# Optimization experiments

Measured on AMD Instinct MI355X. Metric: run time of the kernel, lower is better.

The kernel has to match this reference:

```python
import jax, jax.numpy as jnp
import numpy as np

N = 100000        # nodes
E_HALF = 1600000  # directed edges before symmetrization
NFEAT, NHID, NOUT = 512, 256, 64
K = 10            # Chebyshev order


def setup_inputs() -> dict:
    key = jax.random.key(0)
    k_feat, k_src, k_dst, k_w1, k_w2, k_tmp = jax.random.split(key, 6)
    feature = jax.random.normal(k_feat, (N, NFEAT), jnp.float32)
    src = jax.random.randint(k_src, (E_HALF,), 0, N, jnp.int32)
    dst = jax.random.randint(k_dst, (E_HALF,), 0, N, jnp.int32)
    # symmetrize so the adjacency (and hence the normalized Laplacian) is symmetric
    edge_index = jnp.stack([jnp.concatenate([src, dst]), jnp.concatenate([dst, src])])  # [2, 2*E_HALF]
    W1 = jax.random.normal(k_w1, (NHID, NFEAT), jnp.float32) / np.sqrt(NFEAT)
    b1 = jnp.zeros((NHID,), jnp.float32)
    W2 = jax.random.normal(k_w2, (NOUT, NHID), jnp.float32) / np.sqrt(NHID)
    b2 = jnp.zeros((NOUT,), jnp.float32)
    # ChebnetII_prop.temp is initialized to 1.0; jitter so relu/grads are non-trivial
    temp = 1.0 + 0.1 * jax.random.normal(k_tmp, (K + 1,), jnp.float32)
    return {"feature": feature, "W1": W1, "b1": b1, "W2": W2, "b2": b2,
            "temp": temp, "edge_index": edge_index}


def _cheb_coeffs(temp):
    # coe[i] = 2/(K+1) * sum_j relu(temp)[j] * T_i(x_j),  x_j = cos((K-j+0.5)*pi/(K+1))
    # and T_i(cos(theta)) = cos(i*theta)
    coe_tmp = jax.nn.relu(temp)
    j = jnp.arange(K + 1, dtype=temp.dtype)
    theta = (K - j + 0.5) * jnp.pi / (K + 1)          # [K+1]
    i = jnp.arange(K + 1, dtype=temp.dtype)
    T = jnp.cos(i[:, None] * theta[None, :])           # [K+1, K+1] Chebyshev eval table
    return (2.0 / (K + 1)) * (T @ coe_tmp)             # [K+1]


def reference(feature, W1, b1, W2, b2, temp, edge_index):
    # dense MLP part (dropout is identity in eval mode)
    x = jax.nn.relu(feature @ W1.T + b1)               # [N, NHID]
    x = x @ W2.T + b2                                  # [N, NOUT]

    # ChebnetII_prop: propagate with L_tilde = L_sym - I = -D^{-1/2} A D^{-1/2}
    row, col = edge_index[0], edge_index[1]
    w = jnp.ones(row.shape, x.dtype)                   # unit edge weights (binary adjacency)
    deg = jax.ops.segment_sum(w, row, num_segments=N)  # [N]
    dinv = jnp.where(deg > 0, jax.lax.rsqrt(jnp.maximum(deg, 1.0)), 0.0)
    norm = -dinv[row] * w * dinv[col]                  # [E] edge weights of (L - I)

    def prop(v):  # v: [N, NOUT] -> (L - I) @ v via gather/scatter
        return jax.ops.segment_sum(norm[:, None] * v[col], row, num_segments=N)

    coe = _cheb_coeffs(temp)
    Tx0 = x
    Tx1 = prop(x)
    out = coe[0] / 2.0 * Tx0 + coe[1] * Tx1
    for i in range(2, K + 1):                          # Chebyshev recursion (K fixed, small)
        Tx2 = 2.0 * prop(Tx1) - Tx0
        out = out + coe[i] * Tx2
        Tx0, Tx1 = Tx1, Tx2
    return out                                         # [N, NOUT]
```

## Files before the change

### kernel.cpp

```cpp
#include <hip/hip_runtime.h>

#define K_ORDER 10
#define NFEAT 512
#define NHID 256
#define NOUT 64
#define PI_F 3.14159265358979323846f
#define SCAN_CHUNK 2048

typedef __bf16 bf16x8 __attribute__((ext_vector_type(8)));
typedef unsigned short ushort8 __attribute__((ext_vector_type(8)));
typedef float f32x4 __attribute__((ext_vector_type(4)));

__device__ __forceinline__ float bf2f(unsigned short u) {
    union { unsigned int i; float f; } x;
    x.i = ((unsigned int)u) << 16;
    return x.f;
}

__device__ __forceinline__ unsigned short f2bfu(float f) {
    __bf16 h = (__bf16)f;
    return *(unsigned short*)&h;
}

#define GLOAD_LDS16(g, l) __builtin_amdgcn_global_load_lds( \
    (const __attribute__((address_space(1))) void*)(g),     \
    (__attribute__((address_space(3))) void*)(l), 16, 0, 0)

__global__ void detect_kernel(const unsigned short* __restrict__ temp, int* __restrict__ flag) {
    if (threadIdx.x == 0 && blockIdx.x == 0) {
        int cnt = 0;
        for (int i = 0; i < K_ORDER + 1; ++i) {
            unsigned short s = temp[i];
            if (s >= 0x3E00 && s < 0x4080) cnt++;
        }
        flag[0] = (cnt >= 9) ? 1 : 0;
    }
}

__global__ void prep_weights(const void* __restrict__ W1, const void* __restrict__ b1,
                             const void* __restrict__ W2, const void* __restrict__ b2,
                             const int* __restrict__ flag,
                             unsigned short* __restrict__ w1o, float* __restrict__ b1o,
                             unsigned short* __restrict__ w2o, float* __restrict__ b2o) {
    bool isbf = flag[0] != 0;
    int stride = gridDim.x * blockDim.x;
    int i0 = blockIdx.x * blockDim.x + threadIdx.x;
    const int n1 = NHID * NFEAT;
    const int n2 = NOUT * NHID;
    for (int i = i0; i < n1; i += stride)
        w1o[i] = isbf ? ((const unsigned short*)W1)[i] : f2bfu(((const float*)W1)[i]);
    for (int i = i0; i < n2; i += stride)
        w2o[i] = isbf ? ((const unsigned short*)W2)[i] : f2bfu(((const float*)W2)[i]);
    for (int i = i0; i < NHID; i += stride)
        b1o[i] = isbf ? bf2f(((const unsigned short*)b1)[i]) : ((const float*)b1)[i];
    for (int i = i0; i < NOUT; i += stride)
        b2o[i] = isbf ? bf2f(((const unsigned short*)b2)[i]) : ((const float*)b2)[i];
}


__global__ void count_deg_kernel(const int* __restrict__ row, int* __restrict__ deg, int e) {
    int i = blockIdx.x * blockDim.x + threadIdx.x;
    if (i < e) atomicAdd(&deg[row[i]], 1);
}

__global__ void dinv_kernel(const int* __restrict__ deg, float* __restrict__ dinv, int n) {
    int i = blockIdx.x * blockDim.x + threadIdx.x;
    if (i < n) {
        int d = deg[i];
        dinv[i] = (d > 0) ? rsqrtf((float)d) : 0.0f;
    }
}

__global__ __launch_bounds__(256) void partial_sum_kernel(const int* __restrict__ deg,
                                                          int* __restrict__ bsum, int n) {
    __shared__ int ws[4];
    int b = blockIdx.x, t = threadIdx.x;
    int base = b * SCAN_CHUNK + t * 8;
    int s = 0;
    #pragma unroll
    for (int j = 0; j < 8; ++j) { int i = base + j; if (i < n) s += deg[i]; }
    #pragma unroll
    for (int m = 1; m < 64; m <<= 1) s += __shfl_xor(s, m, 64);
    if ((t & 63) == 0) ws[t >> 6] = s;
    __syncthreads();
    if (t == 0) bsum[b] = ws[0] + ws[1] + ws[2] + ws[3];
}

__global__ void scan_small_kernel(const int* __restrict__ bsum, int* __restrict__ boff,
                                  int* __restrict__ rowptr, int nb, int n) {
    int t = threadIdx.x;
    int v = (t < nb) ? bsum[t] : 0;
    int x = v;
    #pragma unroll
    for (int m = 1; m < 64; m <<= 1) { int y = __shfl_up(x, m, 64); if (t >= m) x += y; }
    if (t < nb) boff[t] = x - v;
    if (t == 63) rowptr[n] = x;
}

__global__ __launch_bounds__(256) void scan_apply_kernel(const int* __restrict__ deg,
                                                         const int* __restrict__ boff,
                                                         int* __restrict__ rowptr,
                                                         int* __restrict__ cursor, int n) {
    __shared__ int wtot[4];
    __shared__ int woff_s[4];
    int b = blockIdx.x, t = threadIdx.x;
    int lane = t & 63, wid = t >> 6;
    int base = b * SCAN_CHUNK + t * 8;
    int v[8], s[8];
    int run = 0;
    #pragma unroll
    for (int j = 0; j < 8; ++j) {
        int i = base + j;
        v[j] = (i < n) ? deg[i] : 0;
        run += v[j];
        s[j] = run;
    }
    int tsum = run;
    int x = tsum;
    #pragma unroll
    for (int m = 1; m < 64; m <<= 1) { int y = __shfl_up(x, m, 64); if (lane >= m) x += y; }
    int texcl = x - tsum;
    if (lane == 63) wtot[wid] = x;
    __syncthreads();
    if (t == 0) {
        int r = 0;
        #pragma unroll
        for (int w = 0; w < 4; ++w) { woff_s[w] = r; r += wtot[w]; }
    }
    __syncthreads();
    int ebase = boff[b] + woff_s[wid] + texcl;
    #pragma unroll
    for (int j = 0; j < 8; ++j) {
        int i = base + j;
        if (i < n) { int ex = ebase + s[j] - v[j]; rowptr[i] = ex; cursor[i] = ex; }
    }
}

__global__ void scatter_kernel(const int* __restrict__ row, const int* __restrict__ col,
                               int* __restrict__ cursor, int* __restrict__ cols_s, int e) {
    int i = blockIdx.x * blockDim.x + threadIdx.x;
    if (i < e) {
        int p = atomicAdd(&cursor[row[i]], 1);
        cols_s[p] = col[i];
    }
}


__global__ void coef_kernel(const void* __restrict__ temp, const int* __restrict__ flag,
                            float* __restrict__ coe) {
    int i = threadIdx.x;
    bool isbf = flag[0] != 0;
    if (i <= K_ORDER) {
        float s = 0.0f;
        #pragma unroll
        for (int j = 0; j <= K_ORDER; ++j) {
            float t = isbf ? bf2f(((const unsigned short*)temp)[j]) : ((const float*)temp)[j];
            t = fmaxf(t, 0.0f);
            float theta = ((float)(K_ORDER - j) + 0.5f) * PI_F / (float)(K_ORDER + 1);
            s += cosf((float)i * theta) * t;
        }
        coe[i] = (2.0f / (float)(K_ORDER + 1)) * s;
    }
}


template<int BN, int NBY, bool RELU, bool A_FLAGGED>
__global__ __launch_bounds__(256) void gemm_kernel(
    const void* __restrict__ A, const unsigned short* __restrict__ Bw,
    const float* __restrict__ bias, const int* __restrict__ flag,
    unsigned short* __restrict__ C, int M, int Kdim, int ldc)
{
    constexpr int BM = 128, BK = 32;
    constexpr int FN = BN / 32;
    constexpr int ABUF = A_FLAGGED ? (BM * BK * 4) : (BM * BK * 2);
    constexpr int BBUF = BN * BK * 2;
    __shared__ char lds[2 * ABUF + 2 * BBUF] __attribute__((aligned(16)));

    const int tid = threadIdx.x;
    const int lane = tid & 63, wid = tid >> 6;
    const int bid = blockIdx.x;
    const int by = bid % NBY;
    const int bx = bid / NBY;
    const int row0 = bx * BM;
    const int col0 = by * BN;
    const int wrow = (wid >> 1) * (BM / 2);
    const int wcol = (wid & 1) * (BN / 2);
    const bool af32 = A_FLAGGED ? (flag[0] == 0) : false;

    char* ldsA0 = lds;
    char* ldsB0 = lds + 2 * ABUF;

    auto stage = [&](int buf, int k0) {
        {
            constexpr int PW = (BBUF / 1024) / 4;
            #pragma unroll
            for (int rr = 0; rr < PW; ++rr) {
                int q = rr * 4 + wid;
                int off = q * 1024 + lane * 16;
                int brow = off >> 6;
                int scol = ((off >> 4) & 3) ^ (brow & 3);
                const char* src = (const char*)Bw + (((size_t)(col0 + brow) * Kdim + k0) << 1) + scol * 16;
                GLOAD_LDS16(src, ldsB0 + buf * BBUF + q * 1024);
            }
        }
        if (af32) {
            #pragma unroll
            for (int rr = 0; rr < 4; ++rr) {
                int q = rr * 4 + wid;
                int off = q * 1024 + lane * 16;
                int arow = off >> 7;
                int scol = ((off >> 4) & 7) ^ (arow & 7);
                int grow = row0 + arow; if (grow >= M) grow = M - 1;
                const char* src = (const char*)A + (((size_t)grow * Kdim + k0) << 2) + scol * 16;
                GLOAD_LDS16(src, ldsA0 + buf * ABUF + q * 1024);
            }
        } else {
            #pragma unroll
            for (int rr = 0; rr < 2; ++rr) {
                int q = rr * 4 + wid;
                int off = q * 1024 + lane * 16;
                int arow = off >> 6;
                int scol = ((off >> 4) & 3) ^ (arow & 3);
                int grow = row0 + arow; if (grow >= M) grow = M - 1;
                const char* src = (const char*)A + (((size_t)grow * Kdim + k0) << 1) + scol * 16;
                GLOAD_LDS16(src, ldsA0 + buf * ABUF + q * 1024);
            }
        }
    };

    f32x4 acc[4][FN] = {};

    auto compute = [&](int buf) {
        const char* Ab = ldsA0 + buf * ABUF;
        const char* Bb = ldsB0 + buf * BBUF;
        const int kq = lane >> 4;
        bf16x8 af[4];
        if (af32) {
            #pragma unroll
            for (int mi = 0; mi < 4; ++mi) {
                int aRow = wrow + mi * 16 + (lane & 15);
                int base = aRow * 128 + kq * 32;
                int sw = (aRow & 7) << 4;
                f32x4 lo = *(const f32x4*)(Ab + (base ^ sw));
                f32x4 hi = *(const f32x4*)(Ab + ((base + 16) ^ sw));
                #pragma unroll
                for (int j = 0; j < 4; ++j) { af[mi][j] = (__bf16)lo[j]; af[mi][j + 4] = (__bf16)hi[j]; }
            }
        } else {
            #pragma unroll
            for (int mi = 0; mi < 4; ++mi) {
                int aRow = wrow + mi * 16 + (lane & 15);
                int o = (aRow * 64 + kq * 16) ^ ((aRow & 3) << 4);
                af[mi] = *(const bf16x8*)(Ab + o);
            }
        }
        bf16x8 bfv[FN];
        #pragma unroll
        for (int ni = 0; ni < FN; ++ni) {
            int bRow = wcol + ni * 16 + (lane & 15);
            int o = (bRow * 64 + kq * 16) ^ ((bRow & 3) << 4);
            bfv[ni] = *(const bf16x8*)(Bb + o);
        }
        #pragma unroll
        for (int mi = 0; mi < 4; ++mi)
            #pragma unroll
            for (int ni = 0; ni < FN; ++ni)
                acc[mi][ni] = __builtin_amdgcn_mfma_f32_16x16x32_bf16(af[mi], bfv[ni],
                                                                      acc[mi][ni], 0, 0, 0);
    };

    const int NT = Kdim / BK;
    stage(0, 0);
    __syncthreads();
    int buf = 0;
    for (int t = 0; t < NT; ++t) {
        if (t + 1 < NT) stage(buf ^ 1, (t + 1) * BK);
        compute(buf);
        __syncthreads();
        buf ^= 1;
    }

    #pragma unroll
    for (int mi = 0; mi < 4; ++mi) {
        #pragma unroll
        for (int ni = 0; ni < FN; ++ni) {
            #pragma unroll
            for (int rg = 0; rg < 4; ++rg) {
                int grow = row0 + wrow + mi * 16 + (lane >> 4) * 4 + rg;
                int gcol = col0 + wcol + ni * 16 + (lane & 15);
                if (grow < M) {
                    float vv = acc[mi][ni][rg] + bias[gcol];
                    if (RELU) vv = fmaxf(vv, 0.0f);
                    C[(size_t)grow * ldc + gcol] = f2bfu(vv);
                }
            }
        }
    }
}


__global__ __launch_bounds__(256) void prop_kernel(const unsigned short* __restrict__ vsrc,
                                                   unsigned short* __restrict__ tdst,
                                                   float* __restrict__ outacc,
                                                   const int* __restrict__ rowptr,
                                                   const int* __restrict__ cols,
                                                   const float* __restrict__ dinv,
                                                   const float* __restrict__ coe,
                                                   int mode, int ci, int n) {
    int lane = threadIdx.x & 63;
    int r = blockIdx.x * 4 + (threadIdx.x >> 6);
    if (r >= n) return;
    int fc = lane & 7;
    int sub = lane >> 3;
    int e0 = rowptr[r], e1 = rowptr[r + 1];
    float acc[8] = {};
    for (int e = e0; e < e1; e += 8) {
        int ee = e + sub;
        bool valid = ee < e1;
        int c = valid ? cols[ee] : 0;
        float w = valid ? dinv[c] : 0.0f;
        ushort8 vv = *(const ushort8*)&vsrc[(size_t)c * NOUT + fc * 8];
        #pragma unroll
        for (int j = 0; j < 8; ++j)
            acc[j] = fmaf(w, bf2f(vv[j]), acc[j]);
    }
    #pragma unroll
    for (int m = 8; m < 64; m <<= 1)
        #pragma unroll
        for (int j = 0; j < 8; ++j)
            acc[j] += __shfl_xor(acc[j], m, 64);

    if (lane < 8) {
        float dr = -dinv[r];
        size_t idx = (size_t)r * NOUT + lane * 8;
        float P[8];
        #pragma unroll
        for (int j = 0; j < 8; ++j) P[j] = dr * acc[j];
        if (mode == 0) {
            ushort8 v0 = *(const ushort8*)&vsrc[idx];
            ushort8 hout;
            #pragma unroll
            for (int j = 0; j < 8; ++j) {
                __bf16 h = (__bf16)P[j];
                hout[j] = *(unsigned short*)&h;
            }
            *(ushort8*)&tdst[idx] = hout;
            #pragma unroll
            for (int j = 0; j < 8; ++j)
                outacc[idx + j] = coe[0] * 0.5f * bf2f(v0[j]) + coe[1] * P[j];
        } else {
            ushort8 t0v = *(const ushort8*)&tdst[idx];
            ushort8 hout;
            float t2a[8];
            #pragma unroll
            for (int j = 0; j < 8; ++j) {
                float t2 = 2.0f * P[j] - bf2f(t0v[j]);
                t2a[j] = t2;
                __bf16 h = (__bf16)t2;
                hout[j] = *(unsigned short*)&h;
            }
            *(ushort8*)&tdst[idx] = hout;
            #pragma unroll
            for (int j = 0; j < 8; ++j)
                outacc[idx + j] += coe[ci] * t2a[j];
        }
    }
}

__global__ void convert_kernel(const float* __restrict__ in, const int* __restrict__ flag,
                               void* __restrict__ out, int n) {
    int i = blockIdx.x * blockDim.x + threadIdx.x;
    bool isbf = flag[0] != 0;
    if (i < n) {
        float v = in[i];
        if (isbf) {
            __bf16 h = (__bf16)v;
            ((unsigned short*)out)[i] = *(unsigned short*)&h;
        } else {
            ((float*)out)[i] = v;
        }
    }
}


extern "C" void kernel_launch(void* const* d_in, const int* in_sizes, int n_in,
                              void* d_out, int out_size, void* d_ws, size_t ws_size,
                              hipStream_t stream) {
    const void* feature = d_in[0];
    const void* W1      = d_in[1];
    const void* b1      = d_in[2];
    const void* W2      = d_in[3];
    const void* b2      = d_in[4];
    const void* temp    = d_in[5];
    const int* edge_index = (const int*)d_in[6];

    const int N = in_sizes[0] / NFEAT;
    const int E = in_sizes[6] / 2;
    const int* row = edge_index;
    const int* col = edge_index + E;
    const int nb = (N + SCAN_CHUNK - 1) / SCAN_CHUNK;

    char* base = (char*)d_ws;
    size_t off = 0;
    auto alloc = [&](size_t bytes) -> char* {
        char* p = base + off;
        off = (off + bytes + 255) & ~(size_t)255;
        return p;
    };
    int*   flag   = (int*)  alloc(4);
    float* coe    = (float*)alloc(64);
    int*   bsum   = (int*)  alloc(256);
    int*   boff   = (int*)  alloc(256);
    unsigned short* w1c = (unsigned short*)alloc((size_t)NHID * NFEAT * 2);
    float* b1c    = (float*)alloc(NHID * 4);
    unsigned short* w2c = (unsigned short*)alloc((size_t)NOUT * NHID * 2);
    float* b2c    = (float*)alloc(NOUT * 4);
    float* dinv   = (float*)alloc((size_t)N * 4);
    int*   deg    = (int*)  alloc((size_t)N * 4);
    int*   rowptr = (int*)  alloc((size_t)(N + 1) * 4);
    int*   cursor = (int*)  alloc((size_t)(N + 1) * 4);
    char*  R      = alloc((size_t)N * NHID * 2);
    unsigned short* xhid = (unsigned short*)R;
    int*   colss  = (int*)R;
    float* outacc = (float*)(R + (size_t)E * 4);
    unsigned short* t_a = (unsigned short*)alloc((size_t)N * NOUT * 2);
    unsigned short* t_b = (unsigned short*)alloc((size_t)N * NOUT * 2);

    detect_kernel<<<1, 64, 0, stream>>>((const unsigned short*)temp, flag);
    coef_kernel<<<1, 64, 0, stream>>>(temp, flag, coe);
    prep_weights<<<128, 256, 0, stream>>>(W1, b1, W2, b2, flag, w1c, b1c, w2c, b2c);

    const int nbm = (N + 127) / 128;
    gemm_kernel<128, 2, true, true><<<dim3(nbm * 2), 256, 0, stream>>>(
        feature, w1c, b1c, flag, xhid, N, NFEAT, NHID);
    gemm_kernel<64, 1, false, false><<<dim3(nbm), 256, 0, stream>>>(
        xhid, w2c, b2c, flag, t_a, N, NHID, NOUT);

    hipMemsetAsync(deg, 0, (size_t)N * 4, stream);
    count_deg_kernel<<<(E + 255) / 256, 256, 0, stream>>>(row, deg, E);
    dinv_kernel<<<(N + 255) / 256, 256, 0, stream>>>(deg, dinv, N);
    partial_sum_kernel<<<nb, 256, 0, stream>>>(deg, bsum, N);
    scan_small_kernel<<<1, 64, 0, stream>>>(bsum, boff, rowptr, nb, N);
    scan_apply_kernel<<<nb, 256, 0, stream>>>(deg, boff, rowptr, cursor, N);
    scatter_kernel<<<(E + 255) / 256, 256, 0, stream>>>(row, col, cursor, colss, E);

    int pb = (N + 3) / 4;
    prop_kernel<<<pb, 256, 0, stream>>>(t_a, t_b, outacc, rowptr, colss, dinv, coe, 0, 0, N);
    unsigned short* src = t_b;
    unsigned short* dst = t_a;
    for (int i = 2; i <= K_ORDER; ++i) {
        prop_kernel<<<pb, 256, 0, stream>>>(src, dst, outacc, rowptr, colss, dinv, coe, 1, i, N);
        unsigned short* tmp = src; src = dst; dst = tmp;
    }

    convert_kernel<<<(N * NOUT + 255) / 256, 256, 0, stream>>>(outacc, flag, d_out, N * NOUT);
}
```

Measured before the change: 1.542 ms.

## Partition CSR scatter into 8 row ranges by blockIdx modulo 8

Replaces the single edge scatter with a partitioned version. A tiny kernel binary-searches rowptr to split the rows into 8 equal-edge ranges. Each block handles one range (blockIdx & 7), reads 4 edges with int4 loads, and scatters only edges whose row falls in its range. The intent appears to be keeping each group's atomics and writes local to one region of cursor and cols_s, likely so each lands on a different XCD's L2, with vectorized loads as a second gain. The cost is reading row/col eight times over and one extra launch.

```diff
diff --git a/kernel.cpp b/kernel.cpp
--- a/kernel.cpp
+++ b/kernel.cpp
@@ -136,12 +136,49 @@
     }
 }
 
-__global__ void scatter_kernel(const int* __restrict__ row, const int* __restrict__ col,
-                               int* __restrict__ cursor, int* __restrict__ cols_s, int e) {
-    int i = blockIdx.x * blockDim.x + threadIdx.x;
-    if (i < e) {
-        int p = atomicAdd(&cursor[row[i]], 1);
-        cols_s[p] = col[i];
+__global__ void part_bounds_kernel(const int* __restrict__ rowptr, int* __restrict__ pb,
+                                   int n, int e) {
+    int j = threadIdx.x;
+    if (j > 8) return;
+    if (j == 8) { pb[8] = n; return; }
+    long target = (long)j * e / 8;
+    int lo = 0, hi = n;
+    while (lo < hi) {
+        int mid = (lo + hi) >> 1;
+        if ((long)rowptr[mid] < target) lo = mid + 1; else hi = mid;
+    }
+    pb[j] = lo;
+}
+
+__global__ __launch_bounds__(256) void scatter_part_kernel(
+    const int* __restrict__ row, const int* __restrict__ col,
+    const int* __restrict__ pbounds, int* __restrict__ cursor,
+    int* __restrict__ cols_s, int e) {
+    const int j = blockIdx.x & 7;
+    const int lo = pbounds[j], hi = pbounds[j + 1];
+    const int base = ((blockIdx.x >> 3) * 256 + threadIdx.x) * 4;
+    if (base + 3 < e) {
+        int4 r4 = *(const int4*)(row + base);
+        int4 c4 = *(const int4*)(col + base);
+        #pragma unroll
+        for (int k = 0; k < 4; ++k) {
+            int r = (&r4.x)[k];
+            if (r >= lo && r < hi) {
+                int p = atomicAdd(&cursor[r], 1);
+                cols_s[p] = (&c4.x)[k];
+            }
+        }
+    } else {
+        for (int k = 0; k < 4; ++k) {
+            int i = base + k;
+            if (i < e) {
+                int r = row[i];
+                if (r >= lo && r < hi) {
+                    int p = atomicAdd(&cursor[r], 1);
+                    cols_s[p] = col[i];
+                }
+            }
+        }
     }
 }
 
@@ -411,6 +448,7 @@
     float* coe    = (float*)alloc(64);
     int*   bsum   = (int*)  alloc(256);
     int*   boff   = (int*)  alloc(256);
+    int*   pbounds= (int*)  alloc(64);
     unsigned short* w1c = (unsigned short*)alloc((size_t)NHID * NFEAT * 2);
     float* b1c    = (float*)alloc(NHID * 4);
     unsigned short* w2c = (unsigned short*)alloc((size_t)NOUT * NHID * 2);
@@ -442,7 +480,11 @@
     partial_sum_kernel<<<nb, 256, 0, stream>>>(deg, bsum, N);
     scan_small_kernel<<<1, 64, 0, stream>>>(bsum, boff, rowptr, nb, N);
     scan_apply_kernel<<<nb, 256, 0, stream>>>(deg, boff, rowptr, cursor, N);
-    scatter_kernel<<<(E + 255) / 256, 256, 0, stream>>>(row, col, cursor, colss, E);
+    part_bounds_kernel<<<1, 16, 0, stream>>>(rowptr, pbounds, N, E);
+    {
+        int nch = (E + 1023) / 1024;
+        scatter_part_kernel<<<nch * 8, 256, 0, stream>>>(row, col, pbounds, cursor, colss, E);
+    }
 
     int pb = (N + 3) / 4;
     prop_kernel<<<pb, 256, 0, stream>>>(t_a, t_b, outacc, rowptr, colss, dinv, coe, 0, 0, N);
```

Result: faster. 1.427 ms (-7.5%).
